# Kernel optimization log

Measured on AMD Instinct MI355X. Metric: run time of the kernel, lower is better.

## Reference

```python
import jax, jax.numpy as jnp
import numpy as np

STRIDE = 2
FOLD = 2
EPS_NORM = 1e-12
EPS_GN = 1e-5


def _fold(t, f):
    # 'b c (f1 w) (f2 h) -> (b f1 f2) c w h'
    b, c, W, H = t.shape
    t = t.reshape(b, c, f, W // f, f, H // f)
    return t.transpose(0, 2, 4, 1, 3, 5).reshape(b * f * f, c, W // f, H // f)


def _unfold(t, f, b0):
    # '(b f1 f2) c w h -> b c (f1 w) (f2 h)'
    bf, c, w, h = t.shape
    t = t.reshape(b0, f, f, c, w, h).transpose(0, 3, 1, 4, 2, 5)
    return t.reshape(b0, c, f * w, f * h)


def _avg_pool(t, s):
    # adaptive_avg_pool2d to (W//s, H//s) with divisible dims == s x s mean pool
    b, c, W, H = t.shape
    return t.reshape(b, c, W // s, s, H // s, s).mean(axis=(3, 5))


def _l2norm(t):
    n = jnp.linalg.norm(t, axis=-1, keepdims=True)
    return t / jnp.maximum(n, EPS_NORM)


def setup_inputs() -> dict:
    key = jax.random.key(0)
    ks = jax.random.split(key, 5)
    B, C_in, H, W = 16, 64, 96, 96
    C_out = 128
    x = jax.random.normal(ks[0], (B, C_in, H, W), dtype=jnp.float32)
    w_f = jax.random.normal(ks[1], (C_out, C_in), dtype=jnp.float32) * (1.0 / np.sqrt(C_in))
    b_f = jnp.zeros((C_out,), dtype=jnp.float32)
    w_v = jax.random.normal(ks[2], (C_out, C_in), dtype=jnp.float32) * (1.0 / np.sqrt(C_in))
    b_v = jnp.zeros((C_out,), dtype=jnp.float32)
    w_skip = jax.random.normal(ks[3], (C_out, C_in, 3, 3), dtype=jnp.float32) * (1.0 / np.sqrt(C_in * 9))
    b_skip = jnp.zeros((C_out,), dtype=jnp.float32)
    gamma = jnp.ones((C_out,), dtype=jnp.float32)
    beta = jnp.zeros((C_out,), dtype=jnp.float32)
    return dict(x=x, w_f=w_f, b_f=b_f, w_v=w_v, b_v=b_v,
                w_skip=w_skip, b_skip=b_skip, gamma=gamma, beta=beta)


def reference(x, w_f, b_f, w_v, b_v, w_skip, b_skip, gamma, beta):
    b0 = x.shape[0]
    # skip path: 3x3 conv, stride 2, pad 1
    identity = jax.lax.conv_general_dilated(
        x, w_skip, window_strides=(STRIDE, STRIDE), padding=((1, 1), (1, 1)),
        dimension_numbers=('NCHW', 'OIHW', 'NCHW')) + b_skip[None, :, None, None]
    # 1x1 convs
    value = jnp.einsum('bchw,oc->bohw', x, w_v) + b_v[None, :, None, None]
    feat = jnp.einsum('bchw,oc->bohw', x, w_f) + b_f[None, :, None, None]
    # fold into local windows
    feat = _fold(feat, FOLD)
    value = _fold(value, FOLD)
    bf, c, w, h = feat.shape
    centers = _avg_pool(feat, STRIDE)                       # [bf, c, ww, hh]
    value_centers = _avg_pool(value, STRIDE)                # [bf, c, ww, hh]
    ww, hh = centers.shape[2], centers.shape[3]
    M, N = ww * hh, w * h
    value_centers = value_centers.reshape(bf, c, M).transpose(0, 2, 1)  # [bf, M, c]
    cen = _l2norm(centers.reshape(bf, c, M).transpose(0, 2, 1))         # [bf, M, c]
    pts = _l2norm(feat.reshape(bf, c, N).transpose(0, 2, 1))            # [bf, N, c]
    sim = jnp.einsum('bmc,bnc->bmn', cen, pts)              # [bf, M, N]
    idx = jnp.argmax(sim, axis=1)                           # [bf, N] hard assignment
    value2 = value.reshape(bf, c, N).transpose(0, 2, 1).reshape(bf * N, c)
    seg = (idx + jnp.arange(bf)[:, None] * M).reshape(-1)   # index-offset trick
    pooled = jax.ops.segment_sum(value2, seg, num_segments=bf * M).reshape(bf, M, c)
    counts = jax.ops.segment_sum(jnp.ones((bf * N,), dtype=value2.dtype), seg,
                                 num_segments=bf * M).reshape(bf, M, 1)
    out = (pooled + value_centers) / (counts + 1.0)
    out = out.transpose(0, 2, 1).reshape(bf, c, ww, hh)
    out = _unfold(out, FOLD, b0)                            # [b0, c, W/2, H/2]
    # GroupNorm with 1 group over (C,H,W)
    mu = out.mean(axis=(1, 2, 3), keepdims=True)
    var = out.var(axis=(1, 2, 3), keepdims=True)
    out = (out - mu) / jnp.sqrt(var + EPS_GN)
    out = out * gamma[None, :, None, None] + beta[None, :, None, None]
    return identity + out
```

## Files before the change

### kernel.cpp

```cpp
#include <hip/hip_runtime.h>

typedef _Float16 f16x8 __attribute__((ext_vector_type(8)));
typedef _Float16 f16x4 __attribute__((ext_vector_type(4)));
typedef float f32x4 __attribute__((ext_vector_type(4)));

__global__ __launch_bounds__(256) void k1a_prep(
    const float* __restrict__ x, const float* __restrict__ w_f,
    const float* __restrict__ w_v, const float* __restrict__ w_skip,
    _Float16* __restrict__ xt16, _Float16* __restrict__ xlo16,
    float* __restrict__ xsum,
    _Float16* __restrict__ wfA, _Float16* __restrict__ wfT,
    _Float16* __restrict__ w_v_h, _Float16* __restrict__ wsf)
{
  const int bid = blockIdx.x;
  const int t = threadIdx.x;

  if (bid >= 768) {
    const int wb = bid - 768;
    for (int i = wb * 512 + t; i < wb * 512 + 512; i += 256) {
      int co = i >> 6, c = i & 63;
      float w = w_f[i];
      _Float16 hi = (_Float16)w, lo = (_Float16)(w - (float)hi);
      int laneA = (co & 15) | (((c >> 3) & 3) << 4);
      int jA = c >> 5;
      size_t oA = ((size_t)(co >> 4) * 4) * 512 + (size_t)laneA * 8 + (c & 7);
      wfA[oA + (size_t)jA * 512] = hi;
      wfA[oA + (size_t)(jA + 2) * 512] = lo;
      int laneT = (c & 15) | (((co >> 3) & 3) << 4);
      int jT = co >> 5;
      size_t oT = ((size_t)(c >> 4) * 8) * 512 + (size_t)laneT * 8 + (co & 7);
      wfT[oT + (size_t)jT * 512] = hi;
      wfT[oT + (size_t)(jT + 4) * 512] = lo;
    }
    for (int i = wb * 512 + t; i < wb * 512 + 512; i += 256)
      w_v_h[i] = (_Float16)w_v[i];
    for (int i = wb * 4608 + t; i < wb * 4608 + 4608; i += 256) {
      int co = i / 576, kk = i % 576;
      int dd = kk >> 6, c = kk & 63, dh = dd / 3, dw = dd % 3;
      int mb = co >> 4, ccol = co & 15;
      int ks = kk >> 5, g = (kk >> 3) & 3, e = kk & 7;
      size_t dst = (((size_t)mb * 18 + ks) * 64 + (ccol | (g << 4))) * 8 + e;
      wsf[dst] = (_Float16)w_skip[((co * 64 + c) * 3 + dh) * 3 + dw];
    }
    return;
  }

  const int b = bid / 48, rp = bid % 48;
  const int c = t >> 2, q = t & 3;
  __shared__ __align__(16) _Float16 xst[2 * 96 * 72];
  __shared__ __align__(16) _Float16 xsl[2 * 96 * 72];

  float pool[12];
  #pragma unroll
  for (int p = 0; p < 12; ++p) pool[p] = 0.f;

  #pragma unroll
  for (int r = 0; r < 2; ++r) {
    const float* xr = x + ((size_t)(b * 64 + c) * 96 + 2 * rp + r) * 96 + q * 24;
    #pragma unroll
    for (int j2 = 0; j2 < 6; ++j2) {
      f32x4 v = *(const f32x4*)(xr + j2 * 4);
      #pragma unroll
      for (int u = 0; u < 4; ++u) {
        int C = q * 24 + j2 * 4 + u;
        _Float16 hi = (_Float16)v[u];
        xst[(r * 96 + C) * 72 + c] = hi;
        xsl[(r * 96 + C) * 72 + c] = (_Float16)(v[u] - (float)hi);
        pool[(j2 * 4 + u) >> 1] += v[u];
      }
    }
  }
  {
    const int f1 = rp >= 24 ? 1 : 0, wl = rp - f1 * 24;
    #pragma unroll
    for (int p = 0; p < 12; ++p) {
      int C = q * 24 + 2 * p;
      int f2 = C >= 48 ? 1 : 0;
      int m = wl * 24 + (C - f2 * 48) / 2;
      xsum[((size_t)(b * 4 + f1 * 2 + f2) * 576 + m) * 64 + c] = 0.25f * pool[p];
    }
  }
  __syncthreads();
  for (int i = t; i < 1536; i += 256) {
    int r = i / 768, rem = i % 768, col = rem >> 3, cg = rem & 7;
    size_t gdst = (((size_t)b * 96 + 2 * rp + r) * 96 + col) * 64 + cg * 8;
    *(f16x8*)(xt16 + gdst) = *(const f16x8*)&xst[(r * 96 + col) * 72 + cg * 8];
    *(f16x8*)(xlo16 + gdst) = *(const f16x8*)&xsl[(r * 96 + col) * 72 + cg * 8];
  }
}

__global__ __launch_bounds__(256) void k1b_centers(
    const float* __restrict__ xsum, const float* __restrict__ b_f,
    const _Float16* __restrict__ wfA, const _Float16* __restrict__ wfT,
    _Float16* __restrict__ cenW, float* __restrict__ dvec)
{
  const int mc = blockIdx.x;
  const int bf = blockIdx.y;
  const int m0 = mc * 96;
  const int t = threadIdx.x;
  const int lane = t & 63, wid = t >> 6;
  const int ccol = lane & 15, g = lane >> 4;

  __shared__ __align__(16) _Float16 cenT_h[96][136];
  __shared__ __align__(16) _Float16 cenT_l[96][136];
  __shared__ __align__(16) _Float16 xcs_h[96][72];
  __shared__ __align__(16) _Float16 xcs_l[96][72];
  float* part = (float*)&xcs_h[0][0];

  for (int i = t; i < 96 * 64; i += 256) {
    int m = i >> 6, c = i & 63;
    float s = xsum[((size_t)bf * 576 + m0 + m) * 64 + c];
    _Float16 hi = (_Float16)s;
    xcs_h[m][c] = hi;
    xcs_l[m][c] = (_Float16)(s - (float)hi);
  }
  __syncthreads();

  f32x4 acc[2][6];
  f32x4 bfv[2];
  #pragma unroll
  for (int cbi = 0; cbi < 2; ++cbi) {
    const int cb = wid + cbi * 4;
    bfv[cbi] = *(const f32x4*)(b_f + cb * 16 + g * 4);
    const _Float16* wa = wfA + (size_t)cb * 2048 + (size_t)lane * 8;
    f16x8 a0h = *(const f16x8*)(wa);
    f16x8 a1h = *(const f16x8*)(wa + 512);
    f16x8 a0l = *(const f16x8*)(wa + 1024);
    f16x8 a1l = *(const f16x8*)(wa + 1536);
    #pragma unroll
    for (int nb = 0; nb < 6; ++nb) {
      const int m = nb * 16 + ccol;
      f16x8 b0h = *(const f16x8*)&xcs_h[m][g * 8];
      f16x8 b1h = *(const f16x8*)&xcs_h[m][32 + g * 8];
      f16x8 b0l = *(const f16x8*)&xcs_l[m][g * 8];
      f16x8 b1l = *(const f16x8*)&xcs_l[m][32 + g * 8];
      f32x4 a2 = bfv[cbi];
      a2 = __builtin_amdgcn_mfma_f32_16x16x32_f16(a0h, b0h, a2, 0, 0, 0);
      a2 = __builtin_amdgcn_mfma_f32_16x16x32_f16(a1h, b1h, a2, 0, 0, 0);
      a2 = __builtin_amdgcn_mfma_f32_16x16x32_f16(a0h, b0l, a2, 0, 0, 0);
      a2 = __builtin_amdgcn_mfma_f32_16x16x32_f16(a1h, b1l, a2, 0, 0, 0);
      a2 = __builtin_amdgcn_mfma_f32_16x16x32_f16(a0l, b0h, a2, 0, 0, 0);
      a2 = __builtin_amdgcn_mfma_f32_16x16x32_f16(a1l, b1h, a2, 0, 0, 0);
      acc[cbi][nb] = a2;
    }
  }
  __syncthreads();

  #pragma unroll
  for (int nb = 0; nb < 6; ++nb) {
    float ss = 0.f, db = 0.f;
    #pragma unroll
    for (int cbi = 0; cbi < 2; ++cbi)
      #pragma unroll
      for (int r = 0; r < 4; ++r) {
        float v = acc[cbi][nb][r];
        ss = fmaf(v, v, ss);
        db = fmaf(v, bfv[cbi][r], db);
      }
    #pragma unroll
    for (int off = 16; off <= 32; off <<= 1) {
      ss += __shfl_xor(ss, off, 64);
      db += __shfl_xor(db, off, 64);
    }
    if (lane < 16) {
      part[wid * 96 + nb * 16 + lane] = ss;
      part[384 + wid * 96 + nb * 16 + lane] = db;
    }
  }
  __syncthreads();
  if (t < 96) {
    float ss = part[t] + part[96 + t] + part[192 + t] + part[288 + t];
    float db = part[384 + t] + part[480 + t] + part[576 + t] + part[672 + t];
    float inv = 1.0f / fmaxf(sqrtf(ss), 1e-12f);
    part[768 + t] = inv;
    dvec[bf * 576 + m0 + t] = inv * db;
  }
  __syncthreads();

  #pragma unroll
  for (int nb = 0; nb < 6; ++nb) {
    const int m = nb * 16 + ccol;
    const float inv = part[768 + m];
    #pragma unroll
    for (int cbi = 0; cbi < 2; ++cbi) {
      const int cb = wid + cbi * 4;
      #pragma unroll
      for (int r = 0; r < 4; ++r) {
        float v = acc[cbi][nb][r] * inv;
        _Float16 hi = (_Float16)v;
        cenT_h[m][cb * 16 + g * 4 + r] = hi;
        cenT_l[m][cb * 16 + g * 4 + r] = (_Float16)(v - (float)hi);
      }
    }
  }
  __syncthreads();

  const _Float16* wt = wfT + (size_t)wid * 4096 + (size_t)lane * 8;
  f16x8 tbh[4], tbl[4];
  #pragma unroll
  for (int j2 = 0; j2 < 4; ++j2) {
    tbh[j2] = *(const f16x8*)(wt + j2 * 512);
    tbl[j2] = *(const f16x8*)(wt + (j2 + 4) * 512);
  }
  #pragma unroll 1
  for (int mb = 0; mb < 6; ++mb) {
    f16x8 tah[4], tal[4];
    #pragma unroll
    for (int j2 = 0; j2 < 4; ++j2) {
      tah[j2] = *(const f16x8*)&cenT_h[mb * 16 + ccol][j2 * 32 + g * 8];
      tal[j2] = *(const f16x8*)&cenT_l[mb * 16 + ccol][j2 * 32 + g * 8];
    }
    f32x4 a2 = {0.f, 0.f, 0.f, 0.f};
    #pragma unroll
    for (int j2 = 0; j2 < 4; ++j2) {
      a2 = __builtin_amdgcn_mfma_f32_16x16x32_f16(tah[j2], tbh[j2], a2, 0, 0, 0);
      a2 = __builtin_amdgcn_mfma_f32_16x16x32_f16(tah[j2], tbl[j2], a2, 0, 0, 0);
      a2 = __builtin_amdgcn_mfma_f32_16x16x32_f16(tal[j2], tbh[j2], a2, 0, 0, 0);
    }
    const int c = wid * 16 + ccol;
    const int lane2g = ((c >> 3) & 3) << 4;
    const int j2f = c >> 5, e = c & 7;
    #pragma unroll
    for (int r = 0; r < 4; ++r) {
      float v = a2[r];
      _Float16 hi = (_Float16)v;
      _Float16 lo = (_Float16)(v - (float)hi);
      size_t base = (((size_t)bf * 36 + mc * 6 + mb) * 4) * 512
                  + (size_t)((g * 4 + r) | lane2g) * 8 + e;
      cenW[base + (size_t)j2f * 512] = hi;
      cenW[base + (size_t)(j2f + 2) * 512] = lo;
    }
  }
}

__global__ __launch_bounds__(256, 4) void k2_assign(
    const _Float16* __restrict__ xt16, const _Float16* __restrict__ xlo16,
    const _Float16* __restrict__ cenW,
    const float* __restrict__ dvec,
    float* __restrict__ xsum, float* __restrict__ counts)
{
  const int id = blockIdx.x;
  const int xcd = id & 7;
  const int j = id >> 3;
  const int bf = xcd * 8 + j / 18;
  const int tile = j % 18;
  const int b = bf >> 2, f1 = (bf >> 1) & 1, f2 = bf & 1;
  const int t = threadIdx.x;
  const int lane = t & 63, wid = t >> 6;

  const int tr = tile / 3, tc = tile % 3;
  const int w0 = tr * 8, h0 = tc * 16;

  __shared__ __align__(16) _Float16 xh[128][72];
  __shared__ __align__(16) float dvl[576];
  __shared__ float wbv[4][64];
  __shared__ int   wbi[4][64];
  __shared__ int   idxf[128];
  __shared__ int   olist[128];
  __shared__ int   ocnt;

  if (t == 0) ocnt = 0;
  for (int i = t; i < 576; i += 256) dvl[i] = dvec[bf * 576 + i];

  const size_t tbase = (((size_t)b * 96 + f1 * 48 + w0) * 96 + f2 * 48 + h0) * 64;

  for (int i = t; i < 1024; i += 256) {
    int jj = i >> 3, cg = i & 7;
    f16x8 v = *(const f16x8*)(xt16 + tbase
                + ((size_t)(jj >> 4) * 96 + (jj & 15)) * 64 + cg * 8);
    *(f16x8*)&xh[jj][cg * 8] = v;
  }

  const int ccol = lane & 15;
  const int g = lane >> 4;
  const int half = wid >> 1;
  const int nbh = wid & 1;

  f16x8 Bl0[4], Bl1[4];
  #pragma unroll
  for (int q = 0; q < 4; ++q) {
    const size_t po = tbase + (size_t)(nbh * 4 + q) * 6144 + (size_t)ccol * 64 + g * 8;
    Bl0[q] = *(const f16x8*)(xlo16 + po);
    Bl1[q] = *(const f16x8*)(xlo16 + po + 32);
  }
  __syncthreads();

  f16x8 Bh0[4], Bh1[4];
  #pragma unroll
  for (int q = 0; q < 4; ++q) {
    const int p = (nbh * 4 + q) * 16 + ccol;
    Bh0[q] = *(const f16x8*)&xh[p][g * 8];
    Bh1[q] = *(const f16x8*)&xh[p][32 + g * 8];
  }

  const int mb0 = half * 18;
  const _Float16* abase = cenW + (size_t)bf * 73728 + (size_t)mb0 * 2048
                        + (size_t)lane * 8;

  float bv[4];
  int bi[4];
  #pragma unroll
  for (int q = 0; q < 4; ++q) { bv[q] = -3.0e38f; bi[q] = 0; }

  f16x8 aA0 = *(const f16x8*)(abase);
  f16x8 aA1 = *(const f16x8*)(abase + 512);
  f16x8 aA2 = *(const f16x8*)(abase + 1024);
  f16x8 aA3 = *(const f16x8*)(abase + 1536);
  f16x8 aB0, aB1, aB2, aB3;

#define K2_BODY(kk, A0, A1, A2, A3)                                          \
  {                                                                          \
    const int mb = mb0 + (kk);                                               \
    f32x4 dv4 = *(const f32x4*)&dvl[mb * 16 + g * 4];                        \
    _Pragma("unroll")                                                        \
    for (int q = 0; q < 4; ++q) {                                            \
      f32x4 a4 = dv4;                                                        \
      a4 = __builtin_amdgcn_mfma_f32_16x16x32_f16(A0, Bh0[q], a4, 0, 0, 0);  \
      a4 = __builtin_amdgcn_mfma_f32_16x16x32_f16(A1, Bh1[q], a4, 0, 0, 0);  \
      a4 = __builtin_amdgcn_mfma_f32_16x16x32_f16(A0, Bl0[q], a4, 0, 0, 0);  \
      a4 = __builtin_amdgcn_mfma_f32_16x16x32_f16(A1, Bl1[q], a4, 0, 0, 0);  \
      a4 = __builtin_amdgcn_mfma_f32_16x16x32_f16(A2, Bh0[q], a4, 0, 0, 0);  \
      a4 = __builtin_amdgcn_mfma_f32_16x16x32_f16(A3, Bh1[q], a4, 0, 0, 0);  \
      _Pragma("unroll")                                                      \
      for (int r = 0; r < 4; ++r) {                                          \
        float vv = a4[r];                                                    \
        if (vv > bv[q]) { bv[q] = vv; bi[q] = mb * 16 + g * 4 + r; }         \
      }                                                                      \
    }                                                                        \
  }

  #pragma unroll 1
  for (int k = 0; k < 18; k += 2) {
    const _Float16* nb1 = abase + (size_t)(k + 1) * 2048;
    aB0 = *(const f16x8*)(nb1);
    aB1 = *(const f16x8*)(nb1 + 512);
    aB2 = *(const f16x8*)(nb1 + 1024);
    aB3 = *(const f16x8*)(nb1 + 1536);
    K2_BODY(k, aA0, aA1, aA2, aA3);
    const int kn = (k + 2 < 18) ? (k + 2) : 0;
    const _Float16* nb2 = abase + (size_t)kn * 2048;
    aA0 = *(const f16x8*)(nb2);
    aA1 = *(const f16x8*)(nb2 + 512);
    aA2 = *(const f16x8*)(nb2 + 1024);
    aA3 = *(const f16x8*)(nb2 + 1536);
    K2_BODY(k + 1, aB0, aB1, aB2, aB3);
  }
#undef K2_BODY

  #pragma unroll
  for (int q = 0; q < 4; ++q) {
    float v = bv[q]; int mi = bi[q];
    #pragma unroll
    for (int off = 16; off <= 32; off <<= 1) {
      float ov = __shfl_xor(v, off, 64);
      int   oi = __shfl_xor(mi, off, 64);
      if (ov > v || (ov == v && oi < mi)) { v = ov; mi = oi; }
    }
    if (lane < 16) { wbv[wid][q * 16 + lane] = v; wbi[wid][q * 16 + lane] = mi; }
  }
  __syncthreads();

  if (t < 128) {
    int nbg = t >> 6;
    int s = t & 63;
    float v0 = wbv[nbg][s];     int i0 = wbi[nbg][s];
    float v1 = wbv[nbg + 2][s]; int i1 = wbi[nbg + 2][s];
    int mi = (v1 > v0 || (v1 == v0 && i1 < i0)) ? i1 : i0;
    idxf[t] = mi;
    int own = (tr * 4 + ((t >> 4) >> 1)) * 24 + tc * 8 + ((t & 15) >> 1);
    if (mi != own) { int o = atomicAdd(&ocnt, 1); olist[o] = t; }
  }
  __syncthreads();

  for (int si = 0; si < 8; ++si) {
    const int s = wid * 8 + si;
    const int r = s >> 3, q = s & 7;
    const int m = (tr * 4 + r) * 24 + tc * 8 + q;
    const int p00 = (2 * r) * 16 + 2 * q;
    float sum = 0.f;
    int cnt = 0;
    #pragma unroll
    for (int dp = 0; dp < 4; ++dp) {
      const int p = p00 + (dp >> 1) * 16 + (dp & 1);
      if (idxf[p] == m) { sum += (float)xh[p][lane]; ++cnt; }
    }
    if (cnt > 0) {
      atomicAdd(&xsum[((size_t)bf * 576 + m) * 64 + lane], sum);
      if (lane == 0) atomicAdd(&counts[bf * 576 + m], (float)cnt);
    }
  }

  for (int o = wid; o < ocnt; o += 4) {
    const int p = olist[o];
    const int m = idxf[p];
    atomicAdd(&xsum[((size_t)bf * 576 + m) * 64 + lane], (float)xh[p][lane]);
    if (lane == 0) atomicAdd(&counts[bf * 576 + m], 1.0f);
  }
}

__global__ __launch_bounds__(256) void k2c_pool(
    const float* __restrict__ xsum,
    const float* __restrict__ counts, const _Float16* __restrict__ w_v_h,
    const float* __restrict__ b_v, _Float16* __restrict__ om,
    float* __restrict__ gn_sum, float* __restrict__ gn_ss)
{
  const int chunk = blockIdx.x;
  const int bf = blockIdx.y;
  const int m0 = chunk * 144;
  const int t = threadIdx.x;
  const int lane = t & 63, wid = t >> 6;

  __shared__ __align__(16) _Float16 bh[144][72];
  __shared__ __align__(16) _Float16 bl[144][72];
  __shared__ float rcp_l[144];

  for (int i = t; i < 144 * 64; i += 256) {
    int mq = i >> 6, c = i & 63;
    size_t gdx = ((size_t)bf * 576 + m0 + mq) * 64 + c;
    float s = xsum[gdx];
    _Float16 hi = (_Float16)s;
    bh[mq][c] = hi;
    bl[mq][c] = (_Float16)(s - (float)hi);
  }
  if (t < 144) rcp_l[t] = 1.0f / (counts[bf * 576 + m0 + t] + 1.0f);
  __syncthreads();

  const int ccol = lane & 15, row0 = (lane >> 4) * 4, c0 = (lane >> 4) * 8;
  float sacc = 0.f, ssacc = 0.f;

  #pragma unroll
  for (int cbi = 0; cbi < 2; ++cbi) {
    const int cb = wid + cbi * 4;
    const size_t abase = (size_t)(cb * 16 + ccol) * 64;
    f16x8 a0 = *(const f16x8*)(w_v_h + abase + c0);
    f16x8 a1 = *(const f16x8*)(w_v_h + abase + 32 + c0);
    float bvv[4];
    #pragma unroll
    for (int r = 0; r < 4; ++r) bvv[r] = b_v[cb * 16 + row0 + r];
    for (int nb = 0; nb < 9; ++nb) {
      int mq = nb * 16 + ccol;
      f16x8 bh0 = *(const f16x8*)(&bh[mq][c0]);
      f16x8 bh1 = *(const f16x8*)(&bh[mq][32 + c0]);
      f16x8 bl0 = *(const f16x8*)(&bl[mq][c0]);
      f16x8 bl1 = *(const f16x8*)(&bl[mq][32 + c0]);
      f32x4 a2 = {0.f, 0.f, 0.f, 0.f};
      a2 = __builtin_amdgcn_mfma_f32_16x16x32_f16(a0, bh0, a2, 0, 0, 0);
      a2 = __builtin_amdgcn_mfma_f32_16x16x32_f16(a1, bh1, a2, 0, 0, 0);
      a2 = __builtin_amdgcn_mfma_f32_16x16x32_f16(a0, bl0, a2, 0, 0, 0);
      a2 = __builtin_amdgcn_mfma_f32_16x16x32_f16(a1, bl1, a2, 0, 0, 0);
      float rcp = rcp_l[mq];
      f16x4 o4;
      #pragma unroll
      for (int r = 0; r < 4; ++r) {
        float ov = a2[r] * rcp + bvv[r];
        sacc += ov; ssacc += ov * ov;
        o4[r] = (_Float16)ov;
      }
      *(f16x4*)(om + ((size_t)bf * 576 + m0 + mq) * 128 + cb * 16 + row0) = o4;
    }
  }

  #pragma unroll
  for (int off = 1; off < 64; off <<= 1) {
    sacc += __shfl_xor(sacc, off, 64);
    ssacc += __shfl_xor(ssacc, off, 64);
  }
  __shared__ float rs[4], rss[4];
  if (lane == 0) { rs[wid] = sacc; rss[wid] = ssacc; }
  __syncthreads();
  if (t == 0) {
    atomicAdd(gn_sum + (bf >> 2), rs[0] + rs[1] + rs[2] + rs[3]);
    atomicAdd(gn_ss + (bf >> 2), rss[0] + rss[1] + rss[2] + rss[3]);
  }
}

__global__ __launch_bounds__(256, 4) void k4_final(
    const _Float16* __restrict__ xt16, const _Float16* __restrict__ wsf,
    const float* __restrict__ b_skip, const _Float16* __restrict__ om,
    const float* __restrict__ gn_sum, const float* __restrict__ gn_ss,
    const float* __restrict__ gamma, const float* __restrict__ beta,
    float* __restrict__ out)
{
  const int o2 = blockIdx.x;
  const int b  = blockIdx.y;
  const int t = threadIdx.x;
  const int lane = t & 63, wid = t >> 6;

  __shared__ __align__(16) _Float16 xl[3 * 97 * 64];

  if (t < 96) {
    int rr = t >> 5, h2 = t & 31;
    *(unsigned int*)&xl[(rr * 97) * 64 + h2 * 2] = 0u;
  }
  for (int i = t; i < 2304; i += 256) {
    int rr = i / 768, rem = i % 768, col = rem >> 3, cg = rem & 7;
    int gr = 2 * o2 - 1 + rr;
    f16x8 v = {};
    if (gr >= 0)
      v = *(const f16x8*)(xt16 + (((size_t)b * 96 + gr) * 96 + col) * 64 + cg * 8);
    int colp = col + 1;
    *(f16x8*)&xl[(rr * 97 + colp) * 64 + ((cg ^ (colp & 7)) << 3)] = v;
  }
  __syncthreads();

  const int ccol = lane & 15, g = lane >> 4;
  const int mb0 = wid * 2;

  f32x4 acc[2][3] = {};
  const int o3a = ccol;

  #pragma unroll 1
  for (int kc = 0; kc < 6; ++kc) {
    f16x8 A[2][3];
    #pragma unroll
    for (int m2 = 0; m2 < 2; ++m2)
      #pragma unroll
      for (int kq = 0; kq < 3; ++kq) {
        int ks = kc * 3 + kq;
        A[m2][kq] = *(const f16x8*)(wsf + (((size_t)(mb0 + m2) * 18 + ks) * 64 + lane) * 8);
      }
    #pragma unroll
    for (int nb = 0; nb < 3; ++nb) {
      const int o3 = nb * 16 + o3a;
      f16x8 Bf[3];
      #pragma unroll
      for (int kq = 0; kq < 3; ++kq) {
        int ks = kc * 3 + kq;
        int dd = ks >> 1, dh = dd / 3, dw = dd % 3, ch = ks & 1;
        int colp = 2 * o3 + dw;
        Bf[kq] = *(const f16x8*)&xl[(dh * 97 + colp) * 64
                                    + ((((ch << 2) | g) ^ (colp & 7)) << 3)];
      }
      #pragma unroll
      for (int kq = 0; kq < 3; ++kq) {
        acc[0][nb] = __builtin_amdgcn_mfma_f32_16x16x32_f16(A[0][kq], Bf[kq], acc[0][nb], 0, 0, 0);
        acc[1][nb] = __builtin_amdgcn_mfma_f32_16x16x32_f16(A[1][kq], Bf[kq], acc[1][nb], 0, 0, 0);
      }
    }
  }

  const float Ninv = 1.0f / 294912.0f;
  const float mu = gn_sum[b] * Ninv;
  const float var = gn_ss[b] * Ninv - mu * mu;
  const float istd = rsqrtf(var + 1e-5f);
  const int f1 = o2 / 24, w24 = o2 % 24;

  #pragma unroll
  for (int m2 = 0; m2 < 2; ++m2) {
    const int mb = mb0 + m2;
    #pragma unroll
    for (int nb = 0; nb < 3; ++nb) {
      const int o3 = nb * 16 + o3a;
      const int f2 = o3 / 24, h = o3 % 24;
      const int bf = b * 4 + f1 * 2 + f2;
      const int m = w24 * 24 + h;
      f16x4 o4 = *(const f16x4*)(om + ((size_t)bf * 576 + m) * 128 + mb * 16 + g * 4);
      #pragma unroll
      for (int r = 0; r < 4; ++r) {
        int co = mb * 16 + g * 4 + r;
        float gnv = ((float)o4[r] - mu) * istd * gamma[co] + beta[co];
        out[((size_t)(b * 128 + co) * 48 + o2) * 48 + o3] = acc[m2][nb][r] + b_skip[co] + gnv;
      }
    }
  }
}

extern "C" void kernel_launch(void* const* d_in, const int* in_sizes, int n_in,
                              void* d_out, int out_size, void* d_ws, size_t ws_size,
                              hipStream_t stream) {
  const float* x      = (const float*)d_in[0];
  const float* w_f    = (const float*)d_in[1];
  const float* b_f    = (const float*)d_in[2];
  const float* w_v    = (const float*)d_in[3];
  const float* b_v    = (const float*)d_in[4];
  const float* w_skip = (const float*)d_in[5];
  const float* b_skip = (const float*)d_in[6];
  const float* gamma  = (const float*)d_in[7];
  const float* beta   = (const float*)d_in[8];
  float* out = (float*)d_out;

  char* ws = (char*)d_ws;
  _Float16* cenW   = (_Float16*)(ws);
  _Float16* om     = (_Float16*)(ws);
  float*    dvec   = (float*)(ws + 9437184);
  _Float16* wsf    = (_Float16*)(ws + 9584640);
  _Float16* w_v_h  = (_Float16*)(ws + 9732096);
  float*    xsum   = (float*)(ws + 9748480);
  float*    counts = (float*)(ws + 19185664);
  float*    gn_sum = (float*)(ws + 19333120);
  float*    gn_ss  = (float*)(ws + 19333376);
  _Float16* xt16   = (_Float16*)(ws + 19333632);
  _Float16* wfA    = (_Float16*)(ws + 38208000);
  _Float16* wfT    = (_Float16*)(ws + 38240768);
  _Float16* xlo16  = (_Float16*)(ws + 38273536);

  hipMemsetAsync(ws + 19185664, 0, 147968, stream);

  k1a_prep<<<dim3(784), dim3(256), 0, stream>>>(
      x, w_f, w_v, w_skip, xt16, xlo16, xsum, wfA, wfT, w_v_h, wsf);
  k1b_centers<<<dim3(6, 64), dim3(256), 0, stream>>>(
      xsum, b_f, wfA, wfT, cenW, dvec);
  k2_assign<<<dim3(1152), dim3(256), 0, stream>>>(
      xt16, xlo16, cenW, dvec, xsum, counts);
  k2c_pool<<<dim3(4, 64), dim3(256), 0, stream>>>(
      xsum, counts, w_v_h, b_v, om, gn_sum, gn_ss);
  k4_final<<<dim3(48, 16), dim3(256), 0, stream>>>(
      xt16, wsf, b_skip, om, gn_sum, gn_ss, gamma, beta, out);
}
```

Before: 120.3 us.

## Halve k2_assign point tiles and split centers across all four waves

The assignment kernel now processes 64-point tiles instead of 128, doubling the grid to 2304 blocks. Each of the four waves scans a quarter of the centers (9 blocks of 16) over all 64 points, replacing the old split into two point halves and two center halves. A 4-way argmax reduction merges the per-wave results. The aim is more blocks for occupancy and shorter per-block loops, at the cost of loading each center's A-operand data twice as often overall.

```diff
diff --git a/kernel.cpp b/kernel.cpp
--- a/kernel.cpp
+++ b/kernel.cpp
@@ -242,21 +242,21 @@
   const int id = blockIdx.x;
   const int xcd = id & 7;
   const int j = id >> 3;
-  const int bf = xcd * 8 + j / 18;
-  const int tile = j % 18;
+  const int bf = xcd * 8 + j / 36;
+  const int tile = j % 36;
   const int b = bf >> 2, f1 = (bf >> 1) & 1, f2 = bf & 1;
   const int t = threadIdx.x;
   const int lane = t & 63, wid = t >> 6;
 
   const int tr = tile / 3, tc = tile % 3;
-  const int w0 = tr * 8, h0 = tc * 16;
-
-  __shared__ __align__(16) _Float16 xh[128][72];
+  const int w0 = tr * 4, h0 = tc * 16;
+
+  __shared__ __align__(16) _Float16 xh[64][72];
   __shared__ __align__(16) float dvl[576];
   __shared__ float wbv[4][64];
   __shared__ int   wbi[4][64];
-  __shared__ int   idxf[128];
-  __shared__ int   olist[128];
+  __shared__ int   idxf[64];
+  __shared__ int   olist[64];
   __shared__ int   ocnt;
 
   if (t == 0) ocnt = 0;
@@ -264,7 +264,7 @@
 
   const size_t tbase = (((size_t)b * 96 + f1 * 48 + w0) * 96 + f2 * 48 + h0) * 64;
 
-  for (int i = t; i < 1024; i += 256) {
+  for (int i = t; i < 512; i += 256) {
     int jj = i >> 3, cg = i & 7;
     f16x8 v = *(const f16x8*)(xt16 + tbase
                 + ((size_t)(jj >> 4) * 96 + (jj & 15)) * 64 + cg * 8);
@@ -273,13 +273,11 @@
 
   const int ccol = lane & 15;
   const int g = lane >> 4;
-  const int half = wid >> 1;
-  const int nbh = wid & 1;
 
   f16x8 Bl0[4], Bl1[4];
   #pragma unroll
   for (int q = 0; q < 4; ++q) {
-    const size_t po = tbase + (size_t)(nbh * 4 + q) * 6144 + (size_t)ccol * 64 + g * 8;
+    const size_t po = tbase + (size_t)q * 6144 + (size_t)ccol * 64 + g * 8;
     Bl0[q] = *(const f16x8*)(xlo16 + po);
     Bl1[q] = *(const f16x8*)(xlo16 + po + 32);
   }
@@ -288,12 +286,12 @@
   f16x8 Bh0[4], Bh1[4];
   #pragma unroll
   for (int q = 0; q < 4; ++q) {
-    const int p = (nbh * 4 + q) * 16 + ccol;
+    const int p = q * 16 + ccol;
     Bh0[q] = *(const f16x8*)&xh[p][g * 8];
     Bh1[q] = *(const f16x8*)&xh[p][32 + g * 8];
   }
 
-  const int mb0 = half * 18;
+  const int mb0 = wid * 9;
   const _Float16* abase = cenW + (size_t)bf * 73728 + (size_t)mb0 * 2048
                         + (size_t)lane * 8;
 
@@ -302,11 +300,14 @@
   #pragma unroll
   for (int q = 0; q < 4; ++q) { bv[q] = -3.0e38f; bi[q] = 0; }
 
-  f16x8 aA0 = *(const f16x8*)(abase);
-  f16x8 aA1 = *(const f16x8*)(abase + 512);
-  f16x8 aA2 = *(const f16x8*)(abase + 1024);
-  f16x8 aA3 = *(const f16x8*)(abase + 1536);
-  f16x8 aB0, aB1, aB2, aB3;
+  f16x8 aA0, aA1, aA2, aA3, aB0, aB1, aB2, aB3;
+
+#define LDA_A(kk) { const _Float16* pa_ = abase + (size_t)(kk) * 2048;       \
+    aA0 = *(const f16x8*)(pa_);        aA1 = *(const f16x8*)(pa_ + 512);     \
+    aA2 = *(const f16x8*)(pa_ + 1024); aA3 = *(const f16x8*)(pa_ + 1536); }
+#define LDA_B(kk) { const _Float16* pb_ = abase + (size_t)(kk) * 2048;       \
+    aB0 = *(const f16x8*)(pb_);        aB1 = *(const f16x8*)(pb_ + 512);     \
+    aB2 = *(const f16x8*)(pb_ + 1024); aB3 = *(const f16x8*)(pb_ + 1536); }
 
 #define K2_BODY(kk, A0, A1, A2, A3)                                          \
   {                                                                          \
@@ -329,23 +330,18 @@
     }                                                                        \
   }
 
+  LDA_A(0)
   #pragma unroll 1
-  for (int k = 0; k < 18; k += 2) {
-    const _Float16* nb1 = abase + (size_t)(k + 1) * 2048;
-    aB0 = *(const f16x8*)(nb1);
-    aB1 = *(const f16x8*)(nb1 + 512);
-    aB2 = *(const f16x8*)(nb1 + 1024);
-    aB3 = *(const f16x8*)(nb1 + 1536);
+  for (int k = 0; k < 8; k += 2) {
+    LDA_B(k + 1)
     K2_BODY(k, aA0, aA1, aA2, aA3);
-    const int kn = (k + 2 < 18) ? (k + 2) : 0;
-    const _Float16* nb2 = abase + (size_t)kn * 2048;
-    aA0 = *(const f16x8*)(nb2);
-    aA1 = *(const f16x8*)(nb2 + 512);
-    aA2 = *(const f16x8*)(nb2 + 1024);
-    aA3 = *(const f16x8*)(nb2 + 1536);
+    LDA_A(k + 2)
     K2_BODY(k + 1, aB0, aB1, aB2, aB3);
   }
+  K2_BODY(8, aA0, aA1, aA2, aA3);
 #undef K2_BODY
+#undef LDA_A
+#undef LDA_B
 
   #pragma unroll
   for (int q = 0; q < 4; ++q) {
@@ -360,23 +356,24 @@
   }
   __syncthreads();
 
-  if (t < 128) {
-    int nbg = t >> 6;
-    int s = t & 63;
-    float v0 = wbv[nbg][s];     int i0 = wbi[nbg][s];
-    float v1 = wbv[nbg + 2][s]; int i1 = wbi[nbg + 2][s];
-    int mi = (v1 > v0 || (v1 == v0 && i1 < i0)) ? i1 : i0;
+  if (t < 64) {
+    float v = wbv[0][t]; int mi = wbi[0][t];
+    #pragma unroll
+    for (int w2 = 1; w2 < 4; ++w2) {
+      float ov = wbv[w2][t]; int oi = wbi[w2][t];
+      if (ov > v || (ov == v && oi < mi)) { v = ov; mi = oi; }
+    }
     idxf[t] = mi;
-    int own = (tr * 4 + ((t >> 4) >> 1)) * 24 + tc * 8 + ((t & 15) >> 1);
+    int own = (tr * 2 + ((t >> 4) >> 1)) * 24 + tc * 8 + ((t & 15) >> 1);
     if (mi != own) { int o = atomicAdd(&ocnt, 1); olist[o] = t; }
   }
   __syncthreads();
 
-  for (int si = 0; si < 8; ++si) {
-    const int s = wid * 8 + si;
-    const int r = s >> 3, q = s & 7;
-    const int m = (tr * 4 + r) * 24 + tc * 8 + q;
-    const int p00 = (2 * r) * 16 + 2 * q;
+  for (int si = 0; si < 4; ++si) {
+    const int s = wid * 4 + si;
+    const int r = s >> 3, cq = s & 7;
+    const int m = (tr * 2 + r) * 24 + tc * 8 + cq;
+    const int p00 = (2 * r) * 16 + 2 * cq;
     float sum = 0.f;
     int cnt = 0;
     #pragma unroll
@@ -600,7 +597,7 @@
       x, w_f, w_v, w_skip, xt16, xlo16, xsum, wfA, wfT, w_v_h, wsf);
   k1b_centers<<<dim3(6, 64), dim3(256), 0, stream>>>(
       xsum, b_f, wfA, wfT, cenW, dvec);
-  k2_assign<<<dim3(1152), dim3(256), 0, stream>>>(
+  k2_assign<<<dim3(2304), dim3(256), 0, stream>>>(
       xt16, xlo16, cenW, dvec, xsum, counts);
   k2c_pool<<<dim3(4, 64), dim3(256), 0, stream>>>(
       xsum, counts, w_v_h, b_v, om, gn_sum, gn_ss);
```

Measured after the change: 116.5 us (median of 3 runs). 1.03x faster.
